# Performance work log

Measured on AMD Instinct MI355X. Metric: run time of the kernel, lower is better.

Reference implementation:

```python
import jax, jax.numpy as jnp
import numpy as np

LEN_HIS = 20   # q_len_his: sliding-window history length
DIM_C = 4      # dim_c
H = 64         # GRU hidden = final_mlp_hidden_width
D = 36         # global_graph_width(32) + goal(2) + action(2)
N = 32768      # total timesteps across many episodes


def setup_inputs() -> dict:
    key = jax.random.key(0)
    ks = jax.random.split(key, 8)
    emb = jax.random.normal(ks[0], (N, D), jnp.float32)
    dones = (jax.random.uniform(ks[1], (N, 1)) < 0.02).astype(jnp.int32)
    s = lambda k, shape, fan: jax.random.normal(k, shape, jnp.float32) / np.sqrt(fan).astype(np.float32)
    return {
        "embeddings": emb,
        "W_ih": s(ks[2], (3 * H, D), D),
        "W_hh": s(ks[3], (3 * H, H), H),
        "b_ih": jnp.zeros((3 * H,), jnp.float32),
        "b_hh": jnp.zeros((3 * H,), jnp.float32),
        "W1": s(ks[4], (H, H), H),
        "b1": jnp.zeros((H,), jnp.float32),
        "W2": s(ks[5], (DIM_C, H), H),
        "b2": jnp.zeros((DIM_C,), jnp.float32),
        "dones": dones,
    }


def _his_calculate_c(embeddings, W_ih, W_hh, b_ih, b_hh, W1, b1, W2, b2, dones):
    """Batched/padded version of the ragged sliding-window GRU+MLP loop.

    For each timestep t, the torch code runs the GRU over
    embeddings[max(episode_start, t-L+1) : t+1] from a zero hidden state,
    then applies FinalPredMLP to the final hidden state.
    """
    n = embeddings.shape[0]
    done = dones[:, 0] != 0
    idx = jnp.arange(n)
    # episode_start[t] = (index of most recent done strictly before t) + 1, else 0
    prev_done = jnp.concatenate([jnp.zeros((1,), bool), done[:-1]])
    ep_start = jax.lax.cummax(jnp.where(prev_done, idx, 0))
    win_start = jnp.maximum(ep_start, idx - LEN_HIS + 1)            # [N]

    # padded windows: position l holds embeddings[t - (L-1) + l]
    gidx = idx[:, None] - (LEN_HIS - 1) + jnp.arange(LEN_HIS)[None, :]  # [N, L]
    valid = gidx >= win_start[:, None]                                   # [N, L]
    X = embeddings[jnp.clip(gidx, 0, n - 1)] * valid[..., None]          # [N, L, D]

    def cell(h, inp):
        x, v = inp                      # x: [N, D], v: [N]
        gi = x @ W_ih.T + b_ih          # [N, 3H]
        gh = h @ W_hh.T + b_hh          # [N, 3H]
        ir, iz, inn = jnp.split(gi, 3, axis=-1)
        hr, hz, hnn = jnp.split(gh, 3, axis=-1)
        r = jax.nn.sigmoid(ir + hr)
        z = jax.nn.sigmoid(iz + hz)
        ncand = jnp.tanh(inn + r * hnn)
        h_new = (1.0 - z) * ncand + z * h
        return jnp.where(v[:, None], h_new, h), None

    h0 = jnp.zeros((n, H), embeddings.dtype)
    hT, _ = jax.lax.scan(cell, h0, (jnp.swapaxes(X, 0, 1), valid.T))  # [N, H]

    # FinalPredMLP: Linear(H,H) -> ReLU -> Linear(H, dim_c)
    hid = jax.nn.relu(hT @ W1.T + b1)
    return hid @ W2.T + b2              # [N, dim_c]


def reference(embeddings, W_ih, W_hh, b_ih, b_hh, W1, b1, W2, b2, dones):
    return _his_calculate_c(embeddings, W_ih, W_hh, b_ih, b_hh, W1, b1, W2, b2, dones)
```

## Files before the change

### kernel.cpp

```cpp
#include <hip/hip_runtime.h>

#define NT 32768
#define DI 36
#define HH 64
#define G3 192
#define LH 20
#define SGS 196

#define NLOG2E -1.4426950408889634f
#define TLOG2E 2.8853900817779268f

#define UNION_OFF  27440
#define SFIRST_OFF 39728
#define SMEM_BYTES 39792

typedef __attribute__((ext_vector_type(8))) short bf16x8;
typedef __attribute__((ext_vector_type(4))) float f32x4;
typedef __attribute__((ext_vector_type(4))) int int4v;
union frag_cast { int4v i4; bf16x8 h8; };

__device__ __forceinline__ unsigned f2u(float f) { union { float f; unsigned u; } x; x.f = f; return x.u; }
__device__ __forceinline__ float u2f(unsigned u) { union { float f; unsigned u; } x; x.u = u; return x.f; }
__device__ __forceinline__ unsigned short f2bf_rne(float f) {
    union { float f; unsigned u; } x; x.f = f;
    unsigned r = x.u + 0x7FFFu + ((x.u >> 16) & 1u);
    return (unsigned short)(r >> 16);
}

__global__ __launch_bounds__(64) void prep_kernel(
    const float* __restrict__ W_ih, const float* __restrict__ W_hh,
    const float* __restrict__ W1, int4v* __restrict__ wfrag)
{
    const int b = (int)blockIdx.x;
    const int l = (int)threadIdx.x;
    unsigned short e[8];
    if (b < 72) {
        const int set = b / 24, fb = b % 24;
        const int mt = fb >> 1, kt = fb & 1;
        const int m = mt * 16 + (l & 15);
        const float sc = ((mt >> 2) < 2) ? NLOG2E : TLOG2E;
        const int k0 = kt * 32 + (l >> 4) * 8;
#pragma unroll
        for (int jj = 0; jj < 8; ++jj) {
            const int k = k0 + jj;
            if (set == 2) {
                e[jj] = f2bf_rne(W_hh[(size_t)m * HH + k] * sc);
            } else {
                const float v = (k < DI) ? W_ih[(size_t)m * DI + k] * sc : 0.f;
                const unsigned u = f2u(v);
                if (set == 0) e[jj] = (unsigned short)(u >> 16);
                else          e[jj] = (unsigned short)(f2u(v - u2f(u & 0xFFFF0000u)) >> 16);
            }
        }
    } else {
        const int bb = b - 72;
        const bool is_lo = bb >= 8;
        const int f = bb & 7;
        const int mt = f >> 1, kt = f & 1;
        const int m = mt * 16 + (l & 15);
        const int k0 = kt * 32 + (l >> 4) * 8;
#pragma unroll
        for (int jj = 0; jj < 8; ++jj) {
            const float v = W1[(size_t)m * HH + k0 + jj];
            const unsigned u = f2u(v);
            if (!is_lo) e[jj] = (unsigned short)(u >> 16);
            else        e[jj] = (unsigned short)(f2u(v - u2f(u & 0xFFFF0000u)) >> 16);
        }
    }
    int4v p;
    p.x = e[0] | ((unsigned)e[1] << 16); p.y = e[2] | ((unsigned)e[3] << 16);
    p.z = e[4] | ((unsigned)e[5] << 16); p.w = e[6] | ((unsigned)e[7] << 16);
    wfrag[b * 64 + l] = p;
}

__global__ __launch_bounds__(256, 4) void gru_kernel(
    const float* __restrict__ emb, const int4v* __restrict__ wfrag,
    const float* __restrict__ b_ih, const float* __restrict__ b_hh,
    const float* __restrict__ b1, const float* __restrict__ W2,
    const float* __restrict__ b2, const int* __restrict__ dones,
    float* __restrict__ out)
{
    __shared__ __align__(16) char SMEM[SMEM_BYTES];
    float* const Sg = (float*)SMEM;
    unsigned short* const EmbH = (unsigned short*)(SMEM + UNION_OFF);
    unsigned short* const EmbL = EmbH + 48 * 64;
    unsigned short* const HbB  = (unsigned short*)(SMEM + UNION_OFF);
    unsigned short* const HfH  = (unsigned short*)(SMEM + UNION_OFF);
    unsigned short* const HfL  = HfH + 1152;
    int* const sfirst = (int*)(SMEM + SFIRST_OFF);

    const int tid = threadIdx.x;
    const int lane = tid & 63;
    const int W = tid >> 6;
    const int li = lane & 15;
    const int q = lane >> 4;
    const int blk = ((int)blockIdx.x & 7) * 256 + ((int)blockIdx.x >> 3);
    const int T0 = blk * 16;

    {
        int4v* z = (int4v*)EmbH;
        for (int i = tid; i < 768; i += 256) z[i] = int4v{0, 0, 0, 0};
    }
    if (tid < 16) {
        const int tt = T0 + tid;
        int lo = tt - (LH - 1); if (lo < 0) lo = 0;
        int ws = lo;
        for (int j = lo; j < tt; ++j)
            ws = (dones[j] != 0) ? (j + 1) : ws;
        sfirst[tid] = ws - (tt - (LH - 1));
    }
    __syncthreads();
    for (int i = tid; i < 35 * DI; i += 256) {
        const int r = i / DI, c = i % DI;
        int tt = T0 - (LH - 1) + r; tt = tt < 0 ? 0 : tt;
        const float v = emb[(size_t)tt * DI + c];
        const unsigned u = f2u(v);
        EmbH[r * 64 + c] = (unsigned short)(u >> 16);
        EmbL[r * 64 + c] = (unsigned short)(f2u(v - u2f(u & 0xFFFF0000u)) >> 16);
    }

    bf16x8 aih[3][2], ail[3][2], whh[3][2];
#pragma unroll
    for (int g = 0; g < 3; ++g)
#pragma unroll
        for (int kt = 0; kt < 2; ++kt) {
            const int fb = (4 * g + W) * 2 + kt;
            frag_cast a, b, c;
            a.i4 = wfrag[(0 * 24 + fb) * 64 + lane];
            b.i4 = wfrag[(1 * 24 + fb) * 64 + lane];
            c.i4 = wfrag[(2 * 24 + fb) * 64 + lane];
            aih[g][kt] = a.h8; ail[g][kt] = b.h8; whh[g][kt] = c.h8;
        }

    const int joff = 16 * W + 4 * q;
    f32x4 biasI[3];
#pragma unroll
    for (int g = 0; g < 3; ++g) {
        const float sc = (g < 2) ? NLOG2E : TLOG2E;
        const f32x4 bi = *(const f32x4*)&b_ih[64 * g + joff];
        if (g < 2) {
            const f32x4 bh = *(const f32x4*)&b_hh[64 * g + joff];
#pragma unroll
            for (int rr = 0; rr < 4; ++rr) biasI[g][rr] = (bi[rr] + bh[rr]) * sc;
        } else {
#pragma unroll
            for (int rr = 0; rr < 4; ++rr) biasI[g][rr] = bi[rr] * sc;
        }
    }
    f32x4 bnv;
    {
        const f32x4 b = *(const f32x4*)&b_hh[128 + joff];
#pragma unroll
        for (int rr = 0; rr < 4; ++rr) bnv[rr] = b[rr] * TLOG2E;
    }
    __syncthreads();

#pragma unroll
    for (int nt = 0; nt < 3; ++nt) {
        bf16x8 ebh[2], ebl[2];
#pragma unroll
        for (int kt = 0; kt < 2; ++kt) {
            const int idx = (16 * nt + li) * 64 + 32 * kt + 8 * q;
            ebh[kt] = *(const bf16x8*)&EmbH[idx];
            ebl[kt] = *(const bf16x8*)&EmbL[idx];
        }
#pragma unroll
        for (int g = 0; g < 3; ++g) {
            f32x4 a = biasI[g];
            a = __builtin_amdgcn_mfma_f32_16x16x32_bf16(aih[g][0], ebh[0], a, 0, 0, 0);
            a = __builtin_amdgcn_mfma_f32_16x16x32_bf16(aih[g][1], ebh[1], a, 0, 0, 0);
            a = __builtin_amdgcn_mfma_f32_16x16x32_bf16(ail[g][0], ebh[0], a, 0, 0, 0);
            a = __builtin_amdgcn_mfma_f32_16x16x32_bf16(ail[g][1], ebh[1], a, 0, 0, 0);
            a = __builtin_amdgcn_mfma_f32_16x16x32_bf16(aih[g][0], ebl[0], a, 0, 0, 0);
            a = __builtin_amdgcn_mfma_f32_16x16x32_bf16(aih[g][1], ebl[1], a, 0, 0, 0);
            const int row = 16 * nt + li;
            if (row < 35)
                *(f32x4*)&Sg[row * SGS + 64 * g + joff] = a;
        }
    }
    __syncthreads();
    const int sfr = sfirst[li];

    float h[4] = {0.f, 0.f, 0.f, 0.f};
    f32x4 accR, accZ, accN, ginv;
    f32x4 gvR, gvZ, gvN;

    {
        const float* gp = Sg + li * SGS;
        accR = *(const f32x4*)(gp + joff);
        accZ = *(const f32x4*)(gp + 64 + joff);
        ginv = *(const f32x4*)(gp + 128 + joff);
        accN = bnv;
        const bool valid = (0 >= sfr);
#pragma unroll
        for (int rr = 0; rr < 4; ++rr) {
            const float r  = __builtin_amdgcn_rcpf(1.f + __builtin_amdgcn_exp2f(accR[rr]));
            const float z  = __builtin_amdgcn_rcpf(1.f + __builtin_amdgcn_exp2f(accZ[rr]));
            const float nc = 1.f - 2.f * __builtin_amdgcn_rcpf(1.f + __builtin_amdgcn_exp2f(ginv[rr] + r * accN[rr]));
            h[rr] = valid ? fmaf(z, 0.f - nc, nc) : 0.f;
        }
        uint2 ph;
        ph.x = __builtin_amdgcn_perm(f2u(h[1]), f2u(h[0]), 0x07060302u);
        ph.y = __builtin_amdgcn_perm(f2u(h[3]), f2u(h[2]), 0x07060302u);
        *(uint2*)&HbB[1152 + li * 72 + joff] = ph;
        const float* gq = Sg + (li + 1) * SGS;
        gvR = *(const f32x4*)(gq + joff);
        gvZ = *(const f32x4*)(gq + 64 + joff);
        gvN = *(const f32x4*)(gq + 128 + joff);
    }
    __syncthreads();

#pragma unroll 2
    for (int s = 1; s < LH; ++s) {
        const int rb = s & 1;
        const bf16x8 bh0 = *(const bf16x8*)&HbB[rb * 1152 + li * 72 + 8 * q];
        const bf16x8 bh1 = *(const bf16x8*)&HbB[rb * 1152 + li * 72 + 32 + 8 * q];

        accR = gvR; accZ = gvZ; ginv = gvN; accN = bnv;
        {
            int r = li + s + 1; r = r > 34 ? 34 : r;
            const float* gq = Sg + r * SGS;
            gvR = *(const f32x4*)(gq + joff);
            gvZ = *(const f32x4*)(gq + 64 + joff);
            gvN = *(const f32x4*)(gq + 128 + joff);
        }
#pragma unroll
        for (int g = 0; g < 3; ++g) {
            f32x4 a = (g == 0) ? accR : (g == 1) ? accZ : accN;
            a = __builtin_amdgcn_mfma_f32_16x16x32_bf16(whh[g][0], bh0, a, 0, 0, 0);
            a = __builtin_amdgcn_mfma_f32_16x16x32_bf16(whh[g][1], bh1, a, 0, 0, 0);
            if (g == 0) accR = a; else if (g == 1) accZ = a; else accN = a;
        }
        const bool valid = (s >= sfr);
#pragma unroll
        for (int rr = 0; rr < 4; ++rr) {
            const float r  = __builtin_amdgcn_rcpf(1.f + __builtin_amdgcn_exp2f(accR[rr]));
            const float z  = __builtin_amdgcn_rcpf(1.f + __builtin_amdgcn_exp2f(accZ[rr]));
            const float nc = 1.f - 2.f * __builtin_amdgcn_rcpf(1.f + __builtin_amdgcn_exp2f(ginv[rr] + r * accN[rr]));
            const float hn = fmaf(z, h[rr] - nc, nc);
            h[rr] = valid ? hn : h[rr];
        }
        if (s != LH - 1) {
            uint2 ph;
            ph.x = __builtin_amdgcn_perm(f2u(h[1]), f2u(h[0]), 0x07060302u);
            ph.y = __builtin_amdgcn_perm(f2u(h[3]), f2u(h[2]), 0x07060302u);
            *(uint2*)&HbB[(1 - rb) * 1152 + li * 72 + joff] = ph;
        }
        __syncthreads();
    }

    {
        const unsigned u0 = f2u(h[0]), u1 = f2u(h[1]);
        const unsigned u2 = f2u(h[2]), u3 = f2u(h[3]);
        uint2 ph, pl;
        ph.x = __builtin_amdgcn_perm(u1, u0, 0x07060302u);
        ph.y = __builtin_amdgcn_perm(u3, u2, 0x07060302u);
        const unsigned l0 = f2u(h[0] - u2f(u0 & 0xFFFF0000u));
        const unsigned l1 = f2u(h[1] - u2f(u1 & 0xFFFF0000u));
        const unsigned l2 = f2u(h[2] - u2f(u2 & 0xFFFF0000u));
        const unsigned l3 = f2u(h[3] - u2f(u3 & 0xFFFF0000u));
        pl.x = __builtin_amdgcn_perm(l1, l0, 0x07060302u);
        pl.y = __builtin_amdgcn_perm(l3, l2, 0x07060302u);
        *(uint2*)&HfH[li * 72 + joff] = ph;
        *(uint2*)&HfL[li * 72 + joff] = pl;
    }
    __syncthreads();
    {
        bf16x8 w1h[2], w1l[2];
#pragma unroll
        for (int kt = 0; kt < 2; ++kt) {
            frag_cast a, b;
            a.i4 = wfrag[(72 + W * 2 + kt) * 64 + lane];
            b.i4 = wfrag[(80 + W * 2 + kt) * 64 + lane];
            w1h[kt] = a.h8; w1l[kt] = b.h8;
        }
        const bf16x8 bh0 = *(const bf16x8*)&HfH[li * 72 + 8 * q];
        const bf16x8 bh1 = *(const bf16x8*)&HfH[li * 72 + 32 + 8 * q];
        const bf16x8 bl0 = *(const bf16x8*)&HfL[li * 72 + 8 * q];
        const bf16x8 bl1 = *(const bf16x8*)&HfL[li * 72 + 32 + 8 * q];
        f32x4 a = *(const f32x4*)&b1[joff];
        a = __builtin_amdgcn_mfma_f32_16x16x32_bf16(w1h[0], bh0, a, 0, 0, 0);
        a = __builtin_amdgcn_mfma_f32_16x16x32_bf16(w1h[1], bh1, a, 0, 0, 0);
        a = __builtin_amdgcn_mfma_f32_16x16x32_bf16(w1l[0], bh0, a, 0, 0, 0);
        a = __builtin_amdgcn_mfma_f32_16x16x32_bf16(w1l[1], bh1, a, 0, 0, 0);
        a = __builtin_amdgcn_mfma_f32_16x16x32_bf16(w1h[0], bl0, a, 0, 0, 0);
        a = __builtin_amdgcn_mfma_f32_16x16x32_bf16(w1h[1], bl1, a, 0, 0, 0);
        __syncthreads();
        float4 st;
        st.x = fmaxf(a[0], 0.f); st.y = fmaxf(a[1], 0.f);
        st.z = fmaxf(a[2], 0.f); st.w = fmaxf(a[3], 0.f);
        *(float4*)&Sg[li * 68 + joff] = st;
    }
    __syncthreads();
    if (tid < 64) {
        const int tt = tid >> 2, c = tid & 3;
        float o2 = b2[c];
        for (int m4 = 0; m4 < 16; ++m4) {
            const float4 hv = *(const float4*)&Sg[tt * 68 + 4 * m4];
            const float4 wv = *(const float4*)&W2[c * HH + 4 * m4];
            o2 += hv.x * wv.x + hv.y * wv.y + hv.z * wv.z + hv.w * wv.w;
        }
        out[(size_t)(T0 + tt) * 4 + c] = o2;
    }
}

extern "C" void kernel_launch(void* const* d_in, const int* in_sizes, int n_in,
                              void* d_out, int out_size, void* d_ws, size_t ws_size,
                              hipStream_t stream) {
    const float* emb  = (const float*)d_in[0];
    const float* W_ih = (const float*)d_in[1];
    const float* W_hh = (const float*)d_in[2];
    const float* b_ih = (const float*)d_in[3];
    const float* b_hh = (const float*)d_in[4];
    const float* W1   = (const float*)d_in[5];
    const float* b1   = (const float*)d_in[6];
    const float* W2   = (const float*)d_in[7];
    const float* b2   = (const float*)d_in[8];
    const int*   dn   = (const int*)d_in[9];

    int4v* wfrag = (int4v*)d_ws;
    float* o = (float*)d_out;

    prep_kernel<<<88, 64, 0, stream>>>(W_ih, W_hh, W1, wfrag);
    gru_kernel<<<NT / 16, 256, 0, stream>>>(emb, wfrag, b_ih, b_hh,
                                            b1, W2, b2, dn, o);
}
```

Before: 113.4 us.

## Process 32 timesteps per block with two interleaved recurrence tiles

After: 113.1 us. Within noise of the previous version (-0.2%).

```diff
diff --git a/kernel.cpp b/kernel.cpp
--- a/kernel.cpp
+++ b/kernel.cpp
@@ -3,16 +3,18 @@
 #define NT 32768
 #define DI 36
 #define HH 64
-#define G3 192
 #define LH 20
+#define TPB 32
+#define NROW 51
 #define SGS 196
+#define EMBS 40
 
 #define NLOG2E -1.4426950408889634f
 #define TLOG2E 2.8853900817779268f
 
-#define UNION_OFF  27440
-#define SFIRST_OFF 39728
-#define SMEM_BYTES 39792
+#define UNION_OFF  39984
+#define SFIRST_OFF 49200
+#define SMEM_BYTES 49328
 
 typedef __attribute__((ext_vector_type(8))) short bf16x8;
 typedef __attribute__((ext_vector_type(4))) float f32x4;
@@ -73,7 +75,7 @@
     wfrag[b * 64 + l] = p;
 }
 
-__global__ __launch_bounds__(256, 4) void gru_kernel(
+__global__ __launch_bounds__(256, 3) void gru_kernel(
     const float* __restrict__ emb, const int4v* __restrict__ wfrag,
     const float* __restrict__ b_ih, const float* __restrict__ b_hh,
     const float* __restrict__ b1, const float* __restrict__ W2,
@@ -83,10 +85,10 @@
     __shared__ __align__(16) char SMEM[SMEM_BYTES];
     float* const Sg = (float*)SMEM;
     unsigned short* const EmbH = (unsigned short*)(SMEM + UNION_OFF);
-    unsigned short* const EmbL = EmbH + 48 * 64;
+    unsigned short* const EmbL = EmbH + NROW * EMBS;
     unsigned short* const HbB  = (unsigned short*)(SMEM + UNION_OFF);
     unsigned short* const HfH  = (unsigned short*)(SMEM + UNION_OFF);
-    unsigned short* const HfL  = HfH + 1152;
+    unsigned short* const HfL  = HfH + 2304;
     int* const sfirst = (int*)(SMEM + SFIRST_OFF);
 
     const int tid = threadIdx.x;
@@ -94,14 +96,14 @@
     const int W = tid >> 6;
     const int li = lane & 15;
     const int q = lane >> 4;
-    const int blk = ((int)blockIdx.x & 7) * 256 + ((int)blockIdx.x >> 3);
-    const int T0 = blk * 16;
+    const int blk = ((int)blockIdx.x & 7) * 128 + ((int)blockIdx.x >> 3);
+    const int T0 = blk * TPB;
 
     {
         int4v* z = (int4v*)EmbH;
-        for (int i = tid; i < 768; i += 256) z[i] = int4v{0, 0, 0, 0};
-    }
-    if (tid < 16) {
+        for (int i = tid; i < 510; i += 256) z[i] = int4v{0, 0, 0, 0};
+    }
+    if (tid < TPB) {
         const int tt = T0 + tid;
         int lo = tt - (LH - 1); if (lo < 0) lo = 0;
         int ws = lo;
@@ -110,13 +112,13 @@
         sfirst[tid] = ws - (tt - (LH - 1));
     }
     __syncthreads();
-    for (int i = tid; i < 35 * DI; i += 256) {
+    for (int i = tid; i < NROW * DI; i += 256) {
         const int r = i / DI, c = i % DI;
         int tt = T0 - (LH - 1) + r; tt = tt < 0 ? 0 : tt;
         const float v = emb[(size_t)tt * DI + c];
         const unsigned u = f2u(v);
-        EmbH[r * 64 + c] = (unsigned short)(u >> 16);
-        EmbL[r * 64 + c] = (unsigned short)(f2u(v - u2f(u & 0xFFFF0000u)) >> 16);
+        EmbH[r * EMBS + c] = (unsigned short)(u >> 16);
+        EmbL[r * EMBS + c] = (unsigned short)(f2u(v - u2f(u & 0xFFFF0000u)) >> 16);
     }
 
     bf16x8 aih[3][2], ail[3][2], whh[3][2];
@@ -156,113 +158,128 @@
     __syncthreads();
 
 #pragma unroll
-    for (int nt = 0; nt < 3; ++nt) {
-        bf16x8 ebh[2], ebl[2];
-#pragma unroll
-        for (int kt = 0; kt < 2; ++kt) {
-            const int idx = (16 * nt + li) * 64 + 32 * kt + 8 * q;
-            ebh[kt] = *(const bf16x8*)&EmbH[idx];
-            ebl[kt] = *(const bf16x8*)&EmbL[idx];
+    for (int nt = 0; nt < 4; ++nt) {
+        const int row = ((nt == 3) ? 35 : 16 * nt) + li;
+        bf16x8 ebh0 = *(const bf16x8*)&EmbH[row * EMBS + 8 * q];
+        bf16x8 ebl0 = *(const bf16x8*)&EmbL[row * EMBS + 8 * q];
+        bf16x8 ebh1 = bf16x8{0, 0, 0, 0, 0, 0, 0, 0};
+        bf16x8 ebl1 = bf16x8{0, 0, 0, 0, 0, 0, 0, 0};
+        if (q == 0) {
+            ebh1 = *(const bf16x8*)&EmbH[row * EMBS + 32];
+            ebl1 = *(const bf16x8*)&EmbL[row * EMBS + 32];
         }
 #pragma unroll
         for (int g = 0; g < 3; ++g) {
             f32x4 a = biasI[g];
-            a = __builtin_amdgcn_mfma_f32_16x16x32_bf16(aih[g][0], ebh[0], a, 0, 0, 0);
-            a = __builtin_amdgcn_mfma_f32_16x16x32_bf16(aih[g][1], ebh[1], a, 0, 0, 0);
-            a = __builtin_amdgcn_mfma_f32_16x16x32_bf16(ail[g][0], ebh[0], a, 0, 0, 0);
-            a = __builtin_amdgcn_mfma_f32_16x16x32_bf16(ail[g][1], ebh[1], a, 0, 0, 0);
-            a = __builtin_amdgcn_mfma_f32_16x16x32_bf16(aih[g][0], ebl[0], a, 0, 0, 0);
-            a = __builtin_amdgcn_mfma_f32_16x16x32_bf16(aih[g][1], ebl[1], a, 0, 0, 0);
-            const int row = 16 * nt + li;
-            if (row < 35)
-                *(f32x4*)&Sg[row * SGS + 64 * g + joff] = a;
-        }
-    }
-    __syncthreads();
-    const int sfr = sfirst[li];
-
-    float h[4] = {0.f, 0.f, 0.f, 0.f};
-    f32x4 accR, accZ, accN, ginv;
-    f32x4 gvR, gvZ, gvN;
+            a = __builtin_amdgcn_mfma_f32_16x16x32_bf16(aih[g][0], ebh0, a, 0, 0, 0);
+            a = __builtin_amdgcn_mfma_f32_16x16x32_bf16(aih[g][1], ebh1, a, 0, 0, 0);
+            a = __builtin_amdgcn_mfma_f32_16x16x32_bf16(ail[g][0], ebh0, a, 0, 0, 0);
+            a = __builtin_amdgcn_mfma_f32_16x16x32_bf16(ail[g][1], ebh1, a, 0, 0, 0);
+            a = __builtin_amdgcn_mfma_f32_16x16x32_bf16(aih[g][0], ebl0, a, 0, 0, 0);
+            a = __builtin_amdgcn_mfma_f32_16x16x32_bf16(aih[g][1], ebl1, a, 0, 0, 0);
+            *(f32x4*)&Sg[row * SGS + 64 * g + joff] = a;
+        }
+    }
+    __syncthreads();
+    const int sfr[2] = { sfirst[li], sfirst[16 + li] };
+
+    float h[2][4];
+    f32x4 gv0[2], gv1[2], gv2[2];
 
     {
-        const float* gp = Sg + li * SGS;
-        accR = *(const f32x4*)(gp + joff);
-        accZ = *(const f32x4*)(gp + 64 + joff);
-        ginv = *(const f32x4*)(gp + 128 + joff);
-        accN = bnv;
-        const bool valid = (0 >= sfr);
-#pragma unroll
-        for (int rr = 0; rr < 4; ++rr) {
-            const float r  = __builtin_amdgcn_rcpf(1.f + __builtin_amdgcn_exp2f(accR[rr]));
-            const float z  = __builtin_amdgcn_rcpf(1.f + __builtin_amdgcn_exp2f(accZ[rr]));
-            const float nc = 1.f - 2.f * __builtin_amdgcn_rcpf(1.f + __builtin_amdgcn_exp2f(ginv[rr] + r * accN[rr]));
-            h[rr] = valid ? fmaf(z, 0.f - nc, nc) : 0.f;
-        }
-        uint2 ph;
-        ph.x = __builtin_amdgcn_perm(f2u(h[1]), f2u(h[0]), 0x07060302u);
-        ph.y = __builtin_amdgcn_perm(f2u(h[3]), f2u(h[2]), 0x07060302u);
-        *(uint2*)&HbB[1152 + li * 72 + joff] = ph;
-        const float* gq = Sg + (li + 1) * SGS;
-        gvR = *(const f32x4*)(gq + joff);
-        gvZ = *(const f32x4*)(gq + 64 + joff);
-        gvN = *(const f32x4*)(gq + 128 + joff);
+#pragma unroll
+        for (int nt = 0; nt < 2; ++nt) {
+            const float* gp = Sg + (16 * nt + li) * SGS;
+            const f32x4 aR = *(const f32x4*)(gp + joff);
+            const f32x4 aZ = *(const f32x4*)(gp + 64 + joff);
+            const f32x4 gI = *(const f32x4*)(gp + 128 + joff);
+            const bool valid = (0 >= sfr[nt]);
+#pragma unroll
+            for (int rr = 0; rr < 4; ++rr) {
+                const float r  = __builtin_amdgcn_rcpf(1.f + __builtin_amdgcn_exp2f(aR[rr]));
+                const float z  = __builtin_amdgcn_rcpf(1.f + __builtin_amdgcn_exp2f(aZ[rr]));
+                const float nc = 1.f - 2.f * __builtin_amdgcn_rcpf(1.f + __builtin_amdgcn_exp2f(gI[rr] + r * bnv[rr]));
+                h[nt][rr] = valid ? fmaf(z, 0.f - nc, nc) : 0.f;
+            }
+            uint2 ph;
+            ph.x = __builtin_amdgcn_perm(f2u(h[nt][1]), f2u(h[nt][0]), 0x07060302u);
+            ph.y = __builtin_amdgcn_perm(f2u(h[nt][3]), f2u(h[nt][2]), 0x07060302u);
+            *(uint2*)&HbB[2304 + (16 * nt + li) * 72 + joff] = ph;
+            const float* gq = Sg + (16 * nt + li + 1) * SGS;
+            gv0[nt] = *(const f32x4*)(gq + joff);
+            gv1[nt] = *(const f32x4*)(gq + 64 + joff);
+            gv2[nt] = *(const f32x4*)(gq + 128 + joff);
+        }
     }
     __syncthreads();
 
 #pragma unroll 2
     for (int s = 1; s < LH; ++s) {
         const int rb = s & 1;
-        const bf16x8 bh0 = *(const bf16x8*)&HbB[rb * 1152 + li * 72 + 8 * q];
-        const bf16x8 bh1 = *(const bf16x8*)&HbB[rb * 1152 + li * 72 + 32 + 8 * q];
-
-        accR = gvR; accZ = gvZ; ginv = gvN; accN = bnv;
-        {
-            int r = li + s + 1; r = r > 34 ? 34 : r;
+        bf16x8 bh0[2], bh1[2];
+#pragma unroll
+        for (int nt = 0; nt < 2; ++nt) {
+            bh0[nt] = *(const bf16x8*)&HbB[rb * 2304 + (16 * nt + li) * 72 + 8 * q];
+            bh1[nt] = *(const bf16x8*)&HbB[rb * 2304 + (16 * nt + li) * 72 + 32 + 8 * q];
+        }
+        f32x4 aR[2], aZ[2], aN[2], gI[2];
+#pragma unroll
+        for (int nt = 0; nt < 2; ++nt) {
+            aR[nt] = gv0[nt]; aZ[nt] = gv1[nt]; gI[nt] = gv2[nt]; aN[nt] = bnv;
+        }
+#pragma unroll
+        for (int nt = 0; nt < 2; ++nt) {
+            int r = 16 * nt + li + s + 1; r = r > NROW - 1 ? NROW - 1 : r;
             const float* gq = Sg + r * SGS;
-            gvR = *(const f32x4*)(gq + joff);
-            gvZ = *(const f32x4*)(gq + 64 + joff);
-            gvN = *(const f32x4*)(gq + 128 + joff);
-        }
-#pragma unroll
-        for (int g = 0; g < 3; ++g) {
-            f32x4 a = (g == 0) ? accR : (g == 1) ? accZ : accN;
-            a = __builtin_amdgcn_mfma_f32_16x16x32_bf16(whh[g][0], bh0, a, 0, 0, 0);
-            a = __builtin_amdgcn_mfma_f32_16x16x32_bf16(whh[g][1], bh1, a, 0, 0, 0);
-            if (g == 0) accR = a; else if (g == 1) accZ = a; else accN = a;
-        }
-        const bool valid = (s >= sfr);
-#pragma unroll
-        for (int rr = 0; rr < 4; ++rr) {
-            const float r  = __builtin_amdgcn_rcpf(1.f + __builtin_amdgcn_exp2f(accR[rr]));
-            const float z  = __builtin_amdgcn_rcpf(1.f + __builtin_amdgcn_exp2f(accZ[rr]));
-            const float nc = 1.f - 2.f * __builtin_amdgcn_rcpf(1.f + __builtin_amdgcn_exp2f(ginv[rr] + r * accN[rr]));
-            const float hn = fmaf(z, h[rr] - nc, nc);
-            h[rr] = valid ? hn : h[rr];
-        }
-        if (s != LH - 1) {
-            uint2 ph;
-            ph.x = __builtin_amdgcn_perm(f2u(h[1]), f2u(h[0]), 0x07060302u);
-            ph.y = __builtin_amdgcn_perm(f2u(h[3]), f2u(h[2]), 0x07060302u);
-            *(uint2*)&HbB[(1 - rb) * 1152 + li * 72 + joff] = ph;
+            gv0[nt] = *(const f32x4*)(gq + joff);
+            gv1[nt] = *(const f32x4*)(gq + 64 + joff);
+            gv2[nt] = *(const f32x4*)(gq + 128 + joff);
+        }
+#pragma unroll
+        for (int nt = 0; nt < 2; ++nt) {
+            aR[nt] = __builtin_amdgcn_mfma_f32_16x16x32_bf16(whh[0][0], bh0[nt], aR[nt], 0, 0, 0);
+            aR[nt] = __builtin_amdgcn_mfma_f32_16x16x32_bf16(whh[0][1], bh1[nt], aR[nt], 0, 0, 0);
+            aZ[nt] = __builtin_amdgcn_mfma_f32_16x16x32_bf16(whh[1][0], bh0[nt], aZ[nt], 0, 0, 0);
+            aZ[nt] = __builtin_amdgcn_mfma_f32_16x16x32_bf16(whh[1][1], bh1[nt], aZ[nt], 0, 0, 0);
+            aN[nt] = __builtin_amdgcn_mfma_f32_16x16x32_bf16(whh[2][0], bh0[nt], aN[nt], 0, 0, 0);
+            aN[nt] = __builtin_amdgcn_mfma_f32_16x16x32_bf16(whh[2][1], bh1[nt], aN[nt], 0, 0, 0);
+        }
+#pragma unroll
+        for (int nt = 0; nt < 2; ++nt) {
+            const bool valid = (s >= sfr[nt]);
+#pragma unroll
+            for (int rr = 0; rr < 4; ++rr) {
+                const float r  = __builtin_amdgcn_rcpf(1.f + __builtin_amdgcn_exp2f(aR[nt][rr]));
+                const float z  = __builtin_amdgcn_rcpf(1.f + __builtin_amdgcn_exp2f(aZ[nt][rr]));
+                const float nc = 1.f - 2.f * __builtin_amdgcn_rcpf(1.f + __builtin_amdgcn_exp2f(gI[nt][rr] + r * aN[nt][rr]));
+                const float hn = fmaf(z, h[nt][rr] - nc, nc);
+                h[nt][rr] = valid ? hn : h[nt][rr];
+            }
+            if (s != LH - 1) {
+                uint2 ph;
+                ph.x = __builtin_amdgcn_perm(f2u(h[nt][1]), f2u(h[nt][0]), 0x07060302u);
+                ph.y = __builtin_amdgcn_perm(f2u(h[nt][3]), f2u(h[nt][2]), 0x07060302u);
+                *(uint2*)&HbB[(1 - rb) * 2304 + (16 * nt + li) * 72 + joff] = ph;
+            }
         }
         __syncthreads();
     }
 
-    {
-        const unsigned u0 = f2u(h[0]), u1 = f2u(h[1]);
-        const unsigned u2 = f2u(h[2]), u3 = f2u(h[3]);
+#pragma unroll
+    for (int nt = 0; nt < 2; ++nt) {
+        const unsigned u0 = f2u(h[nt][0]), u1 = f2u(h[nt][1]);
+        const unsigned u2 = f2u(h[nt][2]), u3 = f2u(h[nt][3]);
         uint2 ph, pl;
         ph.x = __builtin_amdgcn_perm(u1, u0, 0x07060302u);
         ph.y = __builtin_amdgcn_perm(u3, u2, 0x07060302u);
-        const unsigned l0 = f2u(h[0] - u2f(u0 & 0xFFFF0000u));
-        const unsigned l1 = f2u(h[1] - u2f(u1 & 0xFFFF0000u));
-        const unsigned l2 = f2u(h[2] - u2f(u2 & 0xFFFF0000u));
-        const unsigned l3 = f2u(h[3] - u2f(u3 & 0xFFFF0000u));
+        const unsigned l0 = f2u(h[nt][0] - u2f(u0 & 0xFFFF0000u));
+        const unsigned l1 = f2u(h[nt][1] - u2f(u1 & 0xFFFF0000u));
+        const unsigned l2 = f2u(h[nt][2] - u2f(u2 & 0xFFFF0000u));
+        const unsigned l3 = f2u(h[nt][3] - u2f(u3 & 0xFFFF0000u));
         pl.x = __builtin_amdgcn_perm(l1, l0, 0x07060302u);
         pl.y = __builtin_amdgcn_perm(l3, l2, 0x07060302u);
-        *(uint2*)&HfH[li * 72 + joff] = ph;
-        *(uint2*)&HfL[li * 72 + joff] = pl;
+        *(uint2*)&HfH[(16 * nt + li) * 72 + joff] = ph;
+        *(uint2*)&HfL[(16 * nt + li) * 72 + joff] = pl;
     }
     __syncthreads();
     {
@@ -274,27 +291,32 @@
             b.i4 = wfrag[(80 + W * 2 + kt) * 64 + lane];
             w1h[kt] = a.h8; w1l[kt] = b.h8;
         }
-        const bf16x8 bh0 = *(const bf16x8*)&HfH[li * 72 + 8 * q];
-        const bf16x8 bh1 = *(const bf16x8*)&HfH[li * 72 + 32 + 8 * q];
-        const bf16x8 bl0 = *(const bf16x8*)&HfL[li * 72 + 8 * q];
-        const bf16x8 bl1 = *(const bf16x8*)&HfL[li * 72 + 32 + 8 * q];
-        f32x4 a = *(const f32x4*)&b1[joff];
-        a = __builtin_amdgcn_mfma_f32_16x16x32_bf16(w1h[0], bh0, a, 0, 0, 0);
-        a = __builtin_amdgcn_mfma_f32_16x16x32_bf16(w1h[1], bh1, a, 0, 0, 0);
-        a = __builtin_amdgcn_mfma_f32_16x16x32_bf16(w1l[0], bh0, a, 0, 0, 0);
-        a = __builtin_amdgcn_mfma_f32_16x16x32_bf16(w1l[1], bh1, a, 0, 0, 0);
-        a = __builtin_amdgcn_mfma_f32_16x16x32_bf16(w1h[0], bl0, a, 0, 0, 0);
-        a = __builtin_amdgcn_mfma_f32_16x16x32_bf16(w1h[1], bl1, a, 0, 0, 0);
-        __syncthreads();
-        float4 st;
-        st.x = fmaxf(a[0], 0.f); st.y = fmaxf(a[1], 0.f);
-        st.z = fmaxf(a[2], 0.f); st.w = fmaxf(a[3], 0.f);
-        *(float4*)&Sg[li * 68 + joff] = st;
-    }
-    __syncthreads();
-    if (tid < 64) {
+        const f32x4 bb1 = *(const f32x4*)&b1[joff];
+#pragma unroll
+        for (int nt = 0; nt < 2; ++nt) {
+            const int t = 16 * nt + li;
+            const bf16x8 bh0 = *(const bf16x8*)&HfH[t * 72 + 8 * q];
+            const bf16x8 bh1 = *(const bf16x8*)&HfH[t * 72 + 32 + 8 * q];
+            const bf16x8 bl0 = *(const bf16x8*)&HfL[t * 72 + 8 * q];
+            const bf16x8 bl1 = *(const bf16x8*)&HfL[t * 72 + 32 + 8 * q];
+            f32x4 a = bb1;
+            a = __builtin_amdgcn_mfma_f32_16x16x32_bf16(w1h[0], bh0, a, 0, 0, 0);
+            a = __builtin_amdgcn_mfma_f32_16x16x32_bf16(w1h[1], bh1, a, 0, 0, 0);
+            a = __builtin_amdgcn_mfma_f32_16x16x32_bf16(w1l[0], bh0, a, 0, 0, 0);
+            a = __builtin_amdgcn_mfma_f32_16x16x32_bf16(w1l[1], bh1, a, 0, 0, 0);
+            a = __builtin_amdgcn_mfma_f32_16x16x32_bf16(w1h[0], bl0, a, 0, 0, 0);
+            a = __builtin_amdgcn_mfma_f32_16x16x32_bf16(w1h[1], bl1, a, 0, 0, 0);
+            float4 st;
+            st.x = fmaxf(a[0], 0.f); st.y = fmaxf(a[1], 0.f);
+            st.z = fmaxf(a[2], 0.f); st.w = fmaxf(a[3], 0.f);
+            *(float4*)&Sg[t * 68 + joff] = st;
+        }
+    }
+    __syncthreads();
+    if (tid < 128) {
         const int tt = tid >> 2, c = tid & 3;
         float o2 = b2[c];
+#pragma unroll
         for (int m4 = 0; m4 < 16; ++m4) {
             const float4 hv = *(const float4*)&Sg[tt * 68 + 4 * m4];
             const float4 wv = *(const float4*)&W2[c * HH + 4 * m4];
@@ -322,6 +344,6 @@
     float* o = (float*)d_out;
 
     prep_kernel<<<88, 64, 0, stream>>>(W_ih, W_hh, W1, wfrag);
-    gru_kernel<<<NT / 16, 256, 0, stream>>>(emb, wfrag, b_ih, b_hh,
-                                            b1, W2, b2, dn, o);
+    gru_kernel<<<NT / TPB, 256, 0, stream>>>(emb, wfrag, b_ih, b_hh,
+                                             b1, W2, b2, dn, o);
 }
```
